# Performance work log

Measured on AMD Instinct MI355X. Metric: run time of the kernel, lower is better.

Reference implementation:

```python
import jax, jax.numpy as jnp
import numpy as np

N = 50000      # nodes
E = 800000     # edges
DIN = 256
DH = 256
DOUT = 64


def setup_inputs() -> dict:
    key = jax.random.key(0)
    ks = jax.random.split(key, 8)
    x = jax.random.normal(ks[0], (N, DIN), dtype=jnp.float32)
    edge_index = jax.random.randint(ks[1], (2, E), 0, N, dtype=jnp.int64)
    s = 0.05
    W1 = jax.random.normal(ks[2], (DIN, DH), dtype=jnp.float32) * s
    b1 = jnp.zeros((DH,), dtype=jnp.float32)
    W2 = jax.random.normal(ks[3], (DH, DH), dtype=jnp.float32) * s
    b2 = jnp.zeros((DH,), dtype=jnp.float32)
    W3 = jax.random.normal(ks[4], (DH, DOUT), dtype=jnp.float32) * s
    b3 = jnp.zeros((DOUT,), dtype=jnp.float32)
    return {"x": x, "edge_index": edge_index, "W1": W1, "b1": b1,
            "W2": W2, "b2": b2, "W3": W3, "b3": b3}


def gcn_conv(x, src, dst, deg_inv_sqrt, W, b):
    # x: [N, din] -> [N, dout]. PyG GCNConv: h = D^{-1/2}(A+I)D^{-1/2} (x W) + b
    n = x.shape[0]
    h = x @ W                                   # [N, dout]
    norm = deg_inv_sqrt[src] * deg_inv_sqrt[dst]  # [E+N]
    msgs = h[src] * norm[:, None]               # gather + scale, [E+N, dout]
    out = jax.ops.segment_sum(msgs, dst, num_segments=n)  # scatter-add
    return out + b


def _loops(edge_index, n):
    # add self loops, compute symmetric normalization degrees
    sl = jnp.arange(n, dtype=edge_index.dtype)
    src = jnp.concatenate([edge_index[0], sl])
    dst = jnp.concatenate([edge_index[1], sl])
    deg = jax.ops.segment_sum(jnp.ones_like(dst, dtype=jnp.float32), dst, num_segments=n)
    dis = jnp.where(deg > 0, jax.lax.rsqrt(deg), 0.0)
    return src, dst, dis


def reference(x, edge_index, W1, b1, W2, b2, W3, b3):
    src, dst, dis = _loops(edge_index, x.shape[0])
    h = jax.nn.relu(gcn_conv(x, src, dst, dis, W1, b1))   # dropout: eval no-op
    h = jax.nn.relu(gcn_conv(h, src, dst, dis, W2, b2))
    out = gcn_conv(h, src, dst, dis, W3, b3)              # batch=None -> no pooling
    return out
```

## Files before the change

kernel.cpp:

```cpp
#include <hip/hip_runtime.h>
#include <hip/hip_fp8.h>
#include <cstdint>
#include <cstddef>

typedef unsigned short u16;
typedef _Float16 f16x8 __attribute__((ext_vector_type(8)));
typedef float f32x2 __attribute__((ext_vector_type(2)));
typedef float f32x4 __attribute__((ext_vector_type(4)));

#if defined(__has_builtin)
#if __has_builtin(__builtin_amdgcn_cvt_pk_f32_fp8) && __has_builtin(__builtin_amdgcn_cvt_pk_fp8_f32)
#define FP8_BUILTIN 1
#endif
#endif

__device__ __forceinline__ float h2f(u16 u) {
  return (float)__builtin_bit_cast(_Float16, u);
}
__device__ __forceinline__ u16 f2h(float f) {
  return __builtin_bit_cast(u16, (_Float16)f);
}
__device__ __forceinline__ unsigned pkh(float lo, float hi) {
  return (unsigned)f2h(lo) | ((unsigned)f2h(hi) << 16);
}
__device__ __forceinline__ unsigned char ftofp8(float f) {
#ifdef FP8_BUILTIN
  return (unsigned char)(__builtin_amdgcn_cvt_pk_fp8_f32(f, f, 0, false) & 0xFF);
#else
  return __hip_fp8_e4m3(f).__x;
#endif
}

__device__ __forceinline__ void async16(u16* lds, const u16* g) {
  __builtin_amdgcn_global_load_lds(
      (const __attribute__((address_space(1))) unsigned int*)g,
      (__attribute__((address_space(3))) unsigned int*)lds, 16, 0, 0);
}

__device__ __forceinline__ void fma8p2(f32x2* a2, float d, uint2 p) {
#ifdef FP8_BUILTIN
  f32x2 d2; d2[0] = d; d2[1] = d;
  f32x2 v0 = __builtin_amdgcn_cvt_pk_f32_fp8((int)p.x, false);
  f32x2 v1 = __builtin_amdgcn_cvt_pk_f32_fp8((int)p.x, true);
  f32x2 v2 = __builtin_amdgcn_cvt_pk_f32_fp8((int)p.y, false);
  f32x2 v3 = __builtin_amdgcn_cvt_pk_f32_fp8((int)p.y, true);
  a2[0] += d2 * v0; a2[1] += d2 * v1; a2[2] += d2 * v2; a2[3] += d2 * v3;
#else
  const unsigned char* b = (const unsigned char*)&p;
#pragma unroll
  for (int k = 0; k < 8; ++k) {
    __hip_fp8_e4m3 v; v.__x = b[k];
    a2[k >> 1][k & 1] += d * (float)v;
  }
#endif
}

__device__ __forceinline__ void fma8h(float* a, float d, uint4 p) {
  const u16* q = (const u16*)&p;
#pragma unroll
  for (int k = 0; k < 8; ++k) a[k] += d * h2f(q[k]);
}

__device__ __forceinline__ f16x8 cvt8(const float* p) {
  float4 a = *(const float4*)p;
  float4 b = *(const float4*)(p + 4);
  f16x8 r;
  r[0] = (_Float16)a.x; r[1] = (_Float16)a.y; r[2] = (_Float16)a.z; r[3] = (_Float16)a.w;
  r[4] = (_Float16)b.x; r[5] = (_Float16)b.y; r[6] = (_Float16)b.z; r[7] = (_Float16)b.w;
  return r;
}

__device__ __forceinline__ int wave_is64(const void* ep) {
  const unsigned* p = (const unsigned*)ep;
  const int lane = threadIdx.x & 63;
  unsigned v = p[2 * lane + 1] | p[2 * (lane + 64) + 1];
  unsigned long long bal = __ballot(v != 0u);
  return (bal == 0ull) ? 1 : 0;
}

__device__ __forceinline__ int edge_at(const void* ep, int is64, long long idx) {
  if (is64) return (int)((const long long*)ep)[idx];
  return ((const int*)ep)[idx];
}

#define NCHUNK 256

__global__ void zero_f32(float* p, int n) {
  int i = blockIdx.x * 256 + threadIdx.x;
  if (i < n) p[i] = 0.f;
}

__global__ __launch_bounds__(256) void prep_all(
    const float* __restrict__ W1, u16* __restrict__ wt1,
    const float* __restrict__ W2, u16* __restrict__ wt2,
    const float* __restrict__ W3, u16* __restrict__ wt3,
    const void* __restrict__ ep, int* __restrict__ cnt,
    int E, int N, int DIN, int DH, int DOUT,
    int nb_w1, int nb_w2, int nb_w3) {
  int b = blockIdx.x;
  if (b < nb_w1) {
    int idx = b * 256 + threadIdx.x;
    if (idx < DIN * DH) {
      int n = idx / DIN, k = idx % DIN;
      wt1[idx] = f2h(W1[k * DH + n]);
    }
    return;
  }
  b -= nb_w1;
  if (b < nb_w2) {
    int idx = b * 256 + threadIdx.x;
    if (idx < DH * DH) {
      int n = idx / DH, k = idx % DH;
      wt2[idx] = f2h(W2[k * DH + n]);
    }
    return;
  }
  b -= nb_w2;
  if (b < nb_w3) {
    int idx = b * 256 + threadIdx.x;
    if (idx < DH * DOUT) {
      int n = idx / DH, k = idx % DH;
      wt3[idx] = f2h(W3[k * DOUT + n]);
    }
    return;
  }
  b -= nb_w3;
  {
    __shared__ int h[256];
    h[threadIdx.x] = 0;
    __syncthreads();
    int is64 = wave_is64(ep);
    const int per = (E + NCHUNK - 1) / NCHUNK;
    const int e0 = b * per, e1 = min(e0 + per, E);
    for (int e = e0 + (int)threadIdx.x; e < e1; e += 256) {
      int d = edge_at(ep, is64, (long long)E + e);
      d = min(max(d, 0), N - 1);
      atomicAdd(&h[d >> 8], 1);
    }
    __syncthreads();
    cnt[b * 256 + threadIdx.x] = h[threadIdx.x];
  }
}

__device__ __forceinline__ void bases_in_lds(const int* __restrict__ cnt,
                                             int nbuck, int E, int* bl, int* ws4) {
  const int t = threadIdx.x, lane = t & 63, w = t >> 6;
  int tot = 0;
  if (t < nbuck) {
#pragma unroll 4
    for (int c = 0; c < NCHUNK; ++c) tot += cnt[c * 256 + t];
  }
  int inc = tot;
#pragma unroll
  for (int o = 1; o < 64; o <<= 1) {
    int u = __shfl_up(inc, o, 64);
    if (lane >= o) inc += u;
  }
  if (lane == 63) ws4[w] = inc;
  __syncthreads();
  if (t == 0) {
    int run = 0;
#pragma unroll
    for (int k = 0; k < 4; ++k) { int v = ws4[k]; ws4[k + 4] = run; run += v; }
  }
  __syncthreads();
  bl[t] = ws4[w + 4] + inc - tot;
  if (t == 0) bl[nbuck] = E;
  __syncthreads();
}

__global__ __launch_bounds__(256) void csr_bucket(const void* __restrict__ ep,
                                                  const int* __restrict__ cnt,
                                                  unsigned* __restrict__ tmp,
                                                  int E, int N, int nbuck) {
  __shared__ int bl[257];
  __shared__ int cur[256];
  __shared__ int ws4[8];
  const int chunk = blockIdx.x;
  const int t = threadIdx.x;
  bases_in_lds(cnt, nbuck, E, bl, ws4);
  if (t < nbuck) {
    int partial = 0;
    for (int c = 0; c < chunk; ++c) partial += cnt[c * 256 + t];
    cur[t] = bl[t] + partial;
  }
  __syncthreads();
  int is64 = wave_is64(ep);
  const int per = (E + NCHUNK - 1) / NCHUNK;
  const int e0 = chunk * per, e1 = min(e0 + per, E);
  for (int e = e0 + t; e < e1; e += 256) {
    int s = edge_at(ep, is64, e);
    int d = edge_at(ep, is64, (long long)E + e);
    s = min(max(s, 0), N - 1);
    d = min(max(d, 0), N - 1);
    int pos = atomicAdd(&cur[d >> 8], 1);
    tmp[pos] = ((unsigned)d << 16) | (unsigned)s;
  }
}

__global__ __launch_bounds__(256) void csr_final(const unsigned* __restrict__ tmp,
                                                 const int* __restrict__ cnt,
                                                 int* __restrict__ rp,
                                                 float* __restrict__ dis,
                                                 u16* __restrict__ col,
                                                 int N, int E, int nbuck) {
  __shared__ int bl[257];
  __shared__ int hcnt[256];
  __shared__ int curs[256];
  __shared__ int ws4[8];
  const int b = blockIdx.x;
  const int node0 = b * 256;
  const int t = threadIdx.x, lane = t & 63, w = t >> 6;
  bases_in_lds(cnt, nbuck, E, bl, ws4);
  const int k0 = bl[b], k1 = bl[b + 1];
  hcnt[t] = 0;
  __syncthreads();
  for (int k = k0 + t; k < k1; k += 256)
    atomicAdd(&hcnt[(int)(tmp[k] >> 16) - node0], 1);
  __syncthreads();
  const int v = hcnt[t];
  int inc = v;
#pragma unroll
  for (int o = 1; o < 64; o <<= 1) {
    int u = __shfl_up(inc, o, 64);
    if (lane >= o) inc += u;
  }
  __syncthreads();
  if (lane == 63) ws4[w] = inc;
  __syncthreads();
  if (t == 0) {
    int run = 0;
#pragma unroll
    for (int k = 0; k < 4; ++k) { int vv = ws4[k]; ws4[k + 4] = run; run += vv; }
  }
  __syncthreads();
  const int excl = k0 + ws4[w + 4] + inc - v;
  if (node0 + t < N) {
    rp[node0 + t] = excl;
    dis[node0 + t] = rsqrtf((float)(v + 1));
  }
  if (b == 0 && t == 0) rp[N] = E;
  curs[t] = excl;
  __syncthreads();
  for (int k = k0 + t; k < k1; k += 256) {
    unsigned e = tmp[k];
    int dl = (int)(e >> 16) - node0;
    int pos = atomicAdd(&curs[dl], 1);
    col[pos] = (u16)(e & 0xFFFFu);
  }
}

template <int BN, int OUT8, int A32, int SC>
__global__ __launch_bounds__(256) void gemm_bres(const void* __restrict__ A,
                                                 const u16* __restrict__ Bt,
                                                 void* __restrict__ Cv, int Nt,
                                                 int Nrows) {
  constexpr int K = 256;
  constexpr int NJ = BN / 16;
  constexpr int CH = BN * K / 8;
  __shared__ __align__(16) u16 Bs[BN * K];

  const int tid = threadIdx.x, lane = tid & 63, w = tid >> 6;
  const int bm = blockIdx.x, bn = blockIdx.y;

#pragma unroll
  for (int i = 0; i < CH / 256; ++i) {
    int c = tid + i * 256;
    int ln = c & 63, t2 = c >> 6;
    int ks = t2 & 7, j = t2 >> 3;
    int row = j * 16 + (ln & 15);
    int kk = ks * 32 + (ln >> 4) * 8;
    async16(&Bs[(size_t)c * 8], Bt + (size_t)(bn * BN + row) * K + kk);
  }

  const int r16 = lane & 15, quad = lane >> 4;
  const int m0 = w * 32;

  int row0 = bm * 128 + m0 + r16;
  int row1 = row0 + 16;
  f16x8 aa0[8], aa1[8];
  if (A32) {
    row0 = min(row0, Nrows - 1);
    row1 = min(row1, Nrows - 1);
    const float* A0 = (const float*)A + (size_t)row0 * K + quad * 8;
    const float* A1 = (const float*)A + (size_t)row1 * K + quad * 8;
#pragma unroll
    for (int ks = 0; ks < 8; ++ks) {
      aa0[ks] = cvt8(A0 + ks * 32);
      aa1[ks] = cvt8(A1 + ks * 32);
    }
  } else {
    const u16* A0 = (const u16*)A + (size_t)row0 * K + quad * 8;
    const u16* A1 = (const u16*)A + (size_t)row1 * K + quad * 8;
#pragma unroll
    for (int ks = 0; ks < 8; ++ks) {
      aa0[ks] = *(const f16x8*)(A0 + ks * 32);
      aa1[ks] = *(const f16x8*)(A1 + ks * 32);
    }
  }

  f32x4 acc[2][NJ];
  const f32x4 fzero = {0.f, 0.f, 0.f, 0.f};
#pragma unroll
  for (int i = 0; i < 2; ++i)
#pragma unroll
    for (int j = 0; j < NJ; ++j) acc[i][j] = fzero;

  __syncthreads();

#pragma unroll
  for (int ks = 0; ks < 8; ++ks) {
#pragma unroll
    for (int j = 0; j < NJ; ++j) {
      f16x8 bf = *(const f16x8*)(&Bs[(size_t)((j * 8 + ks) * 64 + lane) * 8]);
      acc[0][j] = __builtin_amdgcn_mfma_f32_16x16x32_f16(aa0[ks], bf, acc[0][j], 0, 0, 0);
      acc[1][j] = __builtin_amdgcn_mfma_f32_16x16x32_f16(aa1[ks], bf, acc[1][j], 0, 0, 0);
    }
  }
#pragma unroll
  for (int i = 0; i < 2; ++i)
#pragma unroll
    for (int j = 0; j < NJ; ++j) {
      int gr = bm * 128 + m0 + i * 16 + quad * 4;
      int gc = bn * BN + j * 16 + r16;
#pragma unroll
      for (int r = 0; r < 4; ++r) {
        if (OUT8) {
          ((unsigned char*)Cv)[(size_t)(gr + r) * Nt + gc] =
              ftofp8(acc[i][j][r] * (float)SC);
        } else {
          ((u16*)Cv)[(size_t)(gr + r) * Nt + gc] = f2h(acc[i][j][r]);
        }
      }
    }
}

template <int SCALED>
__global__ __launch_bounds__(256) void agg_d256(const unsigned char* __restrict__ h,
                                                const int* __restrict__ rp,
                                                const u16* __restrict__ col,
                                                const float* __restrict__ dis,
                                                const float* __restrict__ bias,
                                                u16* __restrict__ out, int N) {
  const int wid = threadIdx.x >> 6, lane = threadIdx.x & 63;
  const int i = blockIdx.x * 4 + wid;
  if (i >= N) return;
  const int sub = lane >> 5;
  const int l32 = lane & 31;
  const int c8 = l32 * 8;
  const float di = dis[i];
  f32x2 a2[4];
#pragma unroll
  for (int k = 0; k < 4; ++k) { a2[k][0] = 0.f; a2[k][1] = 0.f; }
  if (sub == 0) {
    uint2 sv = *(const uint2*)(h + (size_t)i * 256 + c8);
    fma8p2(a2, SCALED ? 1.f : di, sv);
  }
  const int e1 = rp[i + 1];
  for (int base = rp[i]; base < e1; base += 64) {
    int me = base + lane;
    int s_l = 0; float d_l = 0.f;
    if (me < e1) { s_l = (int)col[me]; if (!SCALED) d_l = dis[s_l]; }
    const int cnt = min(64, e1 - base);
    const int cntR = (cnt + 7) & ~7;
    for (int t = 0; t < cntR; t += 8) {
      int sA = __shfl(s_l, t + sub, 64);
      int sB = __shfl(s_l, t + 2 + sub, 64);
      int sC = __shfl(s_l, t + 4 + sub, 64);
      int sD = __shfl(s_l, t + 6 + sub, 64);
      float dA, dB, dC, dD;
      if (SCALED) {
        dA = (t + sub < cnt) ? 1.f : 0.f;
        dB = (t + 2 + sub < cnt) ? 1.f : 0.f;
        dC = (t + 4 + sub < cnt) ? 1.f : 0.f;
        dD = (t + 6 + sub < cnt) ? 1.f : 0.f;
      } else {
        dA = __shfl(d_l, t + sub, 64);
        dB = __shfl(d_l, t + 2 + sub, 64);
        dC = __shfl(d_l, t + 4 + sub, 64);
        dD = __shfl(d_l, t + 6 + sub, 64);
      }
      uint2 pA = *(const uint2*)(h + (size_t)sA * 256 + c8);
      uint2 pB = *(const uint2*)(h + (size_t)sB * 256 + c8);
      uint2 pC = *(const uint2*)(h + (size_t)sC * 256 + c8);
      uint2 pD = *(const uint2*)(h + (size_t)sD * 256 + c8);
      fma8p2(a2, dA, pA); fma8p2(a2, dB, pB);
      fma8p2(a2, dC, pC); fma8p2(a2, dD, pD);
    }
  }
#pragma unroll
  for (int k = 0; k < 4; ++k) {
    a2[k][0] += __shfl_xor(a2[k][0], 32, 64);
    a2[k][1] += __shfl_xor(a2[k][1], 32, 64);
  }
  if (sub == 0) {
    const float inv = SCALED ? 0.25f : 1.f;
    float4 b0 = *(const float4*)(bias + c8);
    float4 b1 = *(const float4*)(bias + c8 + 4);
    float bb[8] = {b0.x, b0.y, b0.z, b0.w, b1.x, b1.y, b1.z, b1.w};
    float r[8];
#pragma unroll
    for (int k = 0; k < 8; ++k)
      r[k] = fmaxf(di * a2[k >> 1][k & 1] * inv + bb[k], 0.f) * di;
    uint4 ov;
    ov.x = pkh(r[0], r[1]); ov.y = pkh(r[2], r[3]);
    ov.z = pkh(r[4], r[5]); ov.w = pkh(r[6], r[7]);
    *(uint4*)(out + (size_t)i * 256 + c8) = ov;
  }
}

__global__ __launch_bounds__(256) void agg_d64(const u16* __restrict__ h,
                                               const int* __restrict__ rp,
                                               const u16* __restrict__ col,
                                               const float* __restrict__ dis,
                                               const float* __restrict__ bias,
                                               float* __restrict__ out, int N) {
  const int wid = threadIdx.x >> 6, lane = threadIdx.x & 63;
  const int i = blockIdx.x * 4 + wid;
  if (i >= N) return;
  const int grp = lane >> 3;
  const int l8 = lane & 7;
  const int c8 = l8 * 8;
  const float di = dis[i];
  float a[8] = {0.f, 0.f, 0.f, 0.f, 0.f, 0.f, 0.f, 0.f};
  if (grp == 0) {
    uint4 sv = *(const uint4*)(h + (size_t)i * 64 + c8);
    fma8h(a, 1.f, sv);
  }
  const int e1 = rp[i + 1];
  for (int base = rp[i]; base < e1; base += 64) {
    int me = base + lane;
    int s_l = 0;
    if (me < e1) s_l = (int)col[me];
    const int cnt = min(64, e1 - base);
    const int cntR = (cnt + 15) & ~15;
    for (int t = 0; t < cntR; t += 16) {
      int sA = __shfl(s_l, t + grp, 64);
      int sB = __shfl(s_l, t + 8 + grp, 64);
      float dA = (t + grp < cnt) ? 1.f : 0.f;
      float dB = (t + 8 + grp < cnt) ? 1.f : 0.f;
      uint4 pA = *(const uint4*)(h + (size_t)sA * 64 + c8);
      uint4 pB = *(const uint4*)(h + (size_t)sB * 64 + c8);
      fma8h(a, dA, pA); fma8h(a, dB, pB);
    }
  }
#pragma unroll
  for (int k = 0; k < 8; ++k) a[k] += __shfl_xor(a[k], 8, 64);
#pragma unroll
  for (int k = 0; k < 8; ++k) a[k] += __shfl_xor(a[k], 16, 64);
#pragma unroll
  for (int k = 0; k < 8; ++k) a[k] += __shfl_xor(a[k], 32, 64);
  if (lane < 8) {
    float4 b0 = *(const float4*)(bias + c8);
    float4 b1 = *(const float4*)(bias + c8 + 4);
    float4 o0, o1;
    o0.x = di * a[0] + b0.x; o0.y = di * a[1] + b0.y;
    o0.z = di * a[2] + b0.z; o0.w = di * a[3] + b0.w;
    o1.x = di * a[4] + b1.x; o1.y = di * a[5] + b1.y;
    o1.z = di * a[6] + b1.z; o1.w = di * a[7] + b1.w;
    *(float4*)(out + (size_t)i * 64 + c8) = o0;
    *(float4*)(out + (size_t)i * 64 + c8 + 4) = o1;
  }
}

extern "C" void kernel_launch(void* const* d_in, const int* in_sizes, int n_in,
                              void* d_out, int out_size, void* d_ws, size_t ws_size,
                              hipStream_t stream) {
  if (n_in < 8) return;
  const float* x = (const float*)d_in[0];
  const void* eptr = d_in[1];
  const float* W1 = (const float*)d_in[2];
  const float* b1 = (const float*)d_in[3];
  const float* W2 = (const float*)d_in[4];
  const float* b2 = (const float*)d_in[5];
  const float* W3 = (const float*)d_in[6];
  const float* b3 = (const float*)d_in[7];
  float* out = (float*)d_out;

  const int DIN = 256, DH = 256;
  const int N = in_sizes[0] / DIN;
  const int E = in_sizes[1] / 2;
  const int DOUT = in_sizes[6] / DH;
  const int MT = (N + 127) / 128;
  const int Mpad = MT * 128;
  const int nbuck = (N + 255) >> 8;

  auto rnd = [](size_t b) { return (b + 255) & ~(size_t)255; };
  size_t required = 0;
  required += rnd((size_t)Mpad * DH * 2);
  required += rnd((size_t)Mpad * DH);
  required += rnd((size_t)E * 2);
  required += rnd((size_t)E * 4);
  required += rnd((size_t)(N + 1) * 4);
  required += rnd((size_t)N * 4);
  required += rnd((size_t)DIN * DH * 2);
  required += rnd((size_t)DH * DH * 2);
  required += rnd((size_t)DH * DOUT * 2);
  required += rnd((size_t)256 * NCHUNK * 4);
  if (ws_size < required || N > 65536 || nbuck > 256 || nbuck < 1 ||
      E < 128 || DOUT != 64) {
    zero_f32<<<(out_size + 255) / 256, 256, 0, stream>>>(out, out_size);
    return;
  }

  char* ws = (char*)d_ws;
  size_t off0 = 0;
  auto alloc = [&](size_t bytes) {
    char* p = ws + off0;
    off0 = (off0 + bytes + 255) & ~(size_t)255;
    return p;
  };
  u16* xpad = (u16*)alloc((size_t)Mpad * DH * 2);
  unsigned char* hbuf = (unsigned char*)alloc((size_t)Mpad * DH);
  u16* colb = (u16*)alloc((size_t)E * 2);
  unsigned* tmpb = (unsigned*)alloc((size_t)E * 4);
  int* rp = (int*)alloc((size_t)(N + 1) * 4);
  float* dis = (float*)alloc((size_t)N * 4);
  u16* wt1 = (u16*)alloc((size_t)DIN * DH * 2);
  u16* wt2 = (u16*)alloc((size_t)DH * DH * 2);
  u16* wt3 = (u16*)alloc((size_t)DH * DOUT * 2);
  int* cnt = (int*)alloc((size_t)256 * NCHUNK * 4);

  const int nb_w1 = (DIN * DH + 255) / 256;
  const int nb_w2 = (DH * DH + 255) / 256;
  const int nb_w3 = (DH * DOUT + 255) / 256;
  prep_all<<<nb_w1 + nb_w2 + nb_w3 + NCHUNK, 256, 0, stream>>>(
      W1, wt1, W2, wt2, W3, wt3, eptr, cnt,
      E, N, DIN, DH, DOUT, nb_w1, nb_w2, nb_w3);

  csr_bucket<<<NCHUNK, 256, 0, stream>>>(eptr, cnt, tmpb, E, N, nbuck);
  csr_final<<<nbuck, 256, 0, stream>>>(tmpb, cnt, rp, dis, colb, N, E, nbuck);

  gemm_bres<128, 1, 1, 1><<<dim3(MT, DH / 128), 256, 0, stream>>>(
      x, wt1, hbuf, DH, N);
  agg_d256<0><<<(N + 3) / 4, 256, 0, stream>>>(hbuf, rp, colb, dis, b1, xpad, N);
  gemm_bres<128, 1, 0, 4><<<dim3(MT, DH / 128), 256, 0, stream>>>(
      xpad, wt2, hbuf, DH, N);
  agg_d256<1><<<(N + 3) / 4, 256, 0, stream>>>(hbuf, rp, colb, dis, b2, xpad, N);
  gemm_bres<64, 0, 0, 1><<<dim3(MT, DOUT / 64), 256, 0, stream>>>(
      xpad, wt3, hbuf, DOUT, N);
  agg_d64<<<(N + 3) / 4, 256, 0, stream>>>((const u16*)hbuf, rp, colb, dis, b3,
                                           out, N);
}
```

Before: 299.7 us.

## Loop GEMM over N tiles per block reusing A fragments; grid-stride aggregation kernels

```diff
diff --git a/kernel.cpp b/kernel.cpp
--- a/kernel.cpp
+++ b/kernel.cpp
@@ -250,32 +250,35 @@
   }
 }
 
-template <int BN, int OUT8, int A32, int SC>
-__global__ __launch_bounds__(256) void gemm_bres(const void* __restrict__ A,
-                                                 const u16* __restrict__ Bt,
-                                                 void* __restrict__ Cv, int Nt,
-                                                 int Nrows) {
+template <int OUT8, int A32, int NBT, int SC>
+__global__ __launch_bounds__(256) void gemm64c(const void* __restrict__ A,
+                                               const u16* __restrict__ Bt,
+                                               void* __restrict__ Cv, int Nt,
+                                               int Nrows) {
   constexpr int K = 256;
-  constexpr int NJ = BN / 16;
+  constexpr int BN = 64;
+  constexpr int NJ = 4;
   constexpr int CH = BN * K / 8;
   __shared__ __align__(16) u16 Bs[BN * K];
 
   const int tid = threadIdx.x, lane = tid & 63, w = tid >> 6;
-  const int bm = blockIdx.x, bn = blockIdx.y;
-
-#pragma unroll
-  for (int i = 0; i < CH / 256; ++i) {
-    int c = tid + i * 256;
-    int ln = c & 63, t2 = c >> 6;
-    int ks = t2 & 7, j = t2 >> 3;
-    int row = j * 16 + (ln & 15);
-    int kk = ks * 32 + (ln >> 4) * 8;
-    async16(&Bs[(size_t)c * 8], Bt + (size_t)(bn * BN + row) * K + kk);
-  }
+  const int bm = blockIdx.x;
+
+  auto stage = [&](int bt) {
+#pragma unroll
+    for (int i = 0; i < CH / 256; ++i) {
+      int c = tid + i * 256;
+      int ln = c & 63, t2 = c >> 6;
+      int ks = t2 & 7, j = t2 >> 3;
+      int row = bt * BN + j * 16 + (ln & 15);
+      int kk = ks * 32 + (ln >> 4) * 8;
+      async16(&Bs[(size_t)c * 8], Bt + (size_t)row * K + kk);
+    }
+  };
+  stage(0);
 
   const int r16 = lane & 15, quad = lane >> 4;
   const int m0 = w * 32;
-
   int row0 = bm * 128 + m0 + r16;
   int row1 = row0 + 16;
   f16x8 aa0[8], aa1[8];
@@ -299,40 +302,44 @@
     }
   }
 
-  f32x4 acc[2][NJ];
   const f32x4 fzero = {0.f, 0.f, 0.f, 0.f};
 #pragma unroll
-  for (int i = 0; i < 2; ++i)
-#pragma unroll
-    for (int j = 0; j < NJ; ++j) acc[i][j] = fzero;
-
-  __syncthreads();
-
-#pragma unroll
-  for (int ks = 0; ks < 8; ++ks) {
-#pragma unroll
-    for (int j = 0; j < NJ; ++j) {
-      f16x8 bf = *(const f16x8*)(&Bs[(size_t)((j * 8 + ks) * 64 + lane) * 8]);
-      acc[0][j] = __builtin_amdgcn_mfma_f32_16x16x32_f16(aa0[ks], bf, acc[0][j], 0, 0, 0);
-      acc[1][j] = __builtin_amdgcn_mfma_f32_16x16x32_f16(aa1[ks], bf, acc[1][j], 0, 0, 0);
-    }
-  }
-#pragma unroll
-  for (int i = 0; i < 2; ++i)
-#pragma unroll
-    for (int j = 0; j < NJ; ++j) {
-      int gr = bm * 128 + m0 + i * 16 + quad * 4;
-      int gc = bn * BN + j * 16 + r16;
-#pragma unroll
-      for (int r = 0; r < 4; ++r) {
-        if (OUT8) {
-          ((unsigned char*)Cv)[(size_t)(gr + r) * Nt + gc] =
-              ftofp8(acc[i][j][r] * (float)SC);
-        } else {
-          ((u16*)Cv)[(size_t)(gr + r) * Nt + gc] = f2h(acc[i][j][r]);
+  for (int bt = 0; bt < NBT; ++bt) {
+    f32x4 acc[2][NJ];
+#pragma unroll
+    for (int i = 0; i < 2; ++i)
+#pragma unroll
+      for (int j = 0; j < NJ; ++j) acc[i][j] = fzero;
+    __syncthreads();
+#pragma unroll
+    for (int ks = 0; ks < 8; ++ks)
+#pragma unroll
+      for (int j = 0; j < NJ; ++j) {
+        f16x8 bf = *(const f16x8*)(&Bs[(size_t)((j * 8 + ks) * 64 + lane) * 8]);
+        acc[0][j] = __builtin_amdgcn_mfma_f32_16x16x32_f16(aa0[ks], bf, acc[0][j], 0, 0, 0);
+        acc[1][j] = __builtin_amdgcn_mfma_f32_16x16x32_f16(aa1[ks], bf, acc[1][j], 0, 0, 0);
+      }
+    if (bt + 1 < NBT) {
+      __syncthreads();
+      stage(bt + 1);
+    }
+#pragma unroll
+    for (int i = 0; i < 2; ++i)
+#pragma unroll
+      for (int j = 0; j < NJ; ++j) {
+        int gr = bm * 128 + m0 + i * 16 + quad * 4;
+        int gc = bt * BN + j * 16 + r16;
+#pragma unroll
+        for (int r = 0; r < 4; ++r) {
+          if (OUT8) {
+            ((unsigned char*)Cv)[(size_t)(gr + r) * Nt + gc] =
+                ftofp8(acc[i][j][r] * (float)SC);
+          } else {
+            ((u16*)Cv)[(size_t)(gr + r) * Nt + gc] = f2h(acc[i][j][r]);
+          }
         }
       }
-    }
+  }
 }
 
 template <int SCALED>
@@ -343,69 +350,70 @@
                                                 const float* __restrict__ bias,
                                                 u16* __restrict__ out, int N) {
   const int wid = threadIdx.x >> 6, lane = threadIdx.x & 63;
-  const int i = blockIdx.x * 4 + wid;
-  if (i >= N) return;
   const int sub = lane >> 5;
   const int l32 = lane & 31;
   const int c8 = l32 * 8;
-  const float di = dis[i];
-  f32x2 a2[4];
-#pragma unroll
-  for (int k = 0; k < 4; ++k) { a2[k][0] = 0.f; a2[k][1] = 0.f; }
-  if (sub == 0) {
-    uint2 sv = *(const uint2*)(h + (size_t)i * 256 + c8);
-    fma8p2(a2, SCALED ? 1.f : di, sv);
-  }
-  const int e1 = rp[i + 1];
-  for (int base = rp[i]; base < e1; base += 64) {
-    int me = base + lane;
-    int s_l = 0; float d_l = 0.f;
-    if (me < e1) { s_l = (int)col[me]; if (!SCALED) d_l = dis[s_l]; }
-    const int cnt = min(64, e1 - base);
-    const int cntR = (cnt + 7) & ~7;
-    for (int t = 0; t < cntR; t += 8) {
-      int sA = __shfl(s_l, t + sub, 64);
-      int sB = __shfl(s_l, t + 2 + sub, 64);
-      int sC = __shfl(s_l, t + 4 + sub, 64);
-      int sD = __shfl(s_l, t + 6 + sub, 64);
-      float dA, dB, dC, dD;
-      if (SCALED) {
-        dA = (t + sub < cnt) ? 1.f : 0.f;
-        dB = (t + 2 + sub < cnt) ? 1.f : 0.f;
-        dC = (t + 4 + sub < cnt) ? 1.f : 0.f;
-        dD = (t + 6 + sub < cnt) ? 1.f : 0.f;
-      } else {
-        dA = __shfl(d_l, t + sub, 64);
-        dB = __shfl(d_l, t + 2 + sub, 64);
-        dC = __shfl(d_l, t + 4 + sub, 64);
-        dD = __shfl(d_l, t + 6 + sub, 64);
+  const int stride = gridDim.x * 4;
+  for (int i = blockIdx.x * 4 + wid; i < N; i += stride) {
+    const float di = dis[i];
+    f32x2 a2[4];
+#pragma unroll
+    for (int k = 0; k < 4; ++k) { a2[k][0] = 0.f; a2[k][1] = 0.f; }
+    if (sub == 0) {
+      uint2 sv = *(const uint2*)(h + (size_t)i * 256 + c8);
+      fma8p2(a2, SCALED ? 1.f : di, sv);
+    }
+    const int e1 = rp[i + 1];
+    for (int base = rp[i]; base < e1; base += 64) {
+      int me = base + lane;
+      int s_l = 0; float d_l = 0.f;
+      if (me < e1) { s_l = (int)col[me]; if (!SCALED) d_l = dis[s_l]; }
+      const int cnt = min(64, e1 - base);
+      const int cntR = (cnt + 7) & ~7;
+      for (int t = 0; t < cntR; t += 8) {
+        int sA = __shfl(s_l, t + sub, 64);
+        int sB = __shfl(s_l, t + 2 + sub, 64);
+        int sC = __shfl(s_l, t + 4 + sub, 64);
+        int sD = __shfl(s_l, t + 6 + sub, 64);
+        float dA, dB, dC, dD;
+        if (SCALED) {
+          dA = (t + sub < cnt) ? 1.f : 0.f;
+          dB = (t + 2 + sub < cnt) ? 1.f : 0.f;
+          dC = (t + 4 + sub < cnt) ? 1.f : 0.f;
+          dD = (t + 6 + sub < cnt) ? 1.f : 0.f;
+        } else {
+          dA = __shfl(d_l, t + sub, 64);
+          dB = __shfl(d_l, t + 2 + sub, 64);
+          dC = __shfl(d_l, t + 4 + sub, 64);
+          dD = __shfl(d_l, t + 6 + sub, 64);
+        }
+        uint2 pA = *(const uint2*)(h + (size_t)sA * 256 + c8);
+        uint2 pB = *(const uint2*)(h + (size_t)sB * 256 + c8);
+        uint2 pC = *(const uint2*)(h + (size_t)sC * 256 + c8);
+        uint2 pD = *(const uint2*)(h + (size_t)sD * 256 + c8);
+        fma8p2(a2, dA, pA); fma8p2(a2, dB, pB);
+        fma8p2(a2, dC, pC); fma8p2(a2, dD, pD);
       }
-      uint2 pA = *(const uint2*)(h + (size_t)sA * 256 + c8);
-      uint2 pB = *(const uint2*)(h + (size_t)sB * 256 + c8);
-      uint2 pC = *(const uint2*)(h + (size_t)sC * 256 + c8);
-      uint2 pD = *(const uint2*)(h + (size_t)sD * 256 + c8);
-      fma8p2(a2, dA, pA); fma8p2(a2, dB, pB);
-      fma8p2(a2, dC, pC); fma8p2(a2, dD, pD);
-    }
-  }
-#pragma unroll
-  for (int k = 0; k < 4; ++k) {
-    a2[k][0] += __shfl_xor(a2[k][0], 32, 64);
-    a2[k][1] += __shfl_xor(a2[k][1], 32, 64);
-  }
-  if (sub == 0) {
-    const float inv = SCALED ? 0.25f : 1.f;
-    float4 b0 = *(const float4*)(bias + c8);
-    float4 b1 = *(const float4*)(bias + c8 + 4);
-    float bb[8] = {b0.x, b0.y, b0.z, b0.w, b1.x, b1.y, b1.z, b1.w};
-    float r[8];
-#pragma unroll
-    for (int k = 0; k < 8; ++k)
-      r[k] = fmaxf(di * a2[k >> 1][k & 1] * inv + bb[k], 0.f) * di;
-    uint4 ov;
-    ov.x = pkh(r[0], r[1]); ov.y = pkh(r[2], r[3]);
-    ov.z = pkh(r[4], r[5]); ov.w = pkh(r[6], r[7]);
-    *(uint4*)(out + (size_t)i * 256 + c8) = ov;
+    }
+#pragma unroll
+    for (int k = 0; k < 4; ++k) {
+      a2[k][0] += __shfl_xor(a2[k][0], 32, 64);
+      a2[k][1] += __shfl_xor(a2[k][1], 32, 64);
+    }
+    if (sub == 0) {
+      const float inv = SCALED ? 0.25f : 1.f;
+      float4 b0 = *(const float4*)(bias + c8);
+      float4 b1 = *(const float4*)(bias + c8 + 4);
+      float bb[8] = {b0.x, b0.y, b0.z, b0.w, b1.x, b1.y, b1.z, b1.w};
+      float r[8];
+#pragma unroll
+      for (int k = 0; k < 8; ++k)
+        r[k] = fmaxf(di * a2[k >> 1][k & 1] * inv + bb[k], 0.f) * di;
+      uint4 ov;
+      ov.x = pkh(r[0], r[1]); ov.y = pkh(r[2], r[3]);
+      ov.z = pkh(r[4], r[5]); ov.w = pkh(r[6], r[7]);
+      *(uint4*)(out + (size_t)i * 256 + c8) = ov;
+    }
   }
 }
 
@@ -416,50 +424,51 @@
                                                const float* __restrict__ bias,
                                                float* __restrict__ out, int N) {
   const int wid = threadIdx.x >> 6, lane = threadIdx.x & 63;
-  const int i = blockIdx.x * 4 + wid;
-  if (i >= N) return;
   const int grp = lane >> 3;
   const int l8 = lane & 7;
   const int c8 = l8 * 8;
-  const float di = dis[i];
-  float a[8] = {0.f, 0.f, 0.f, 0.f, 0.f, 0.f, 0.f, 0.f};
-  if (grp == 0) {
-    uint4 sv = *(const uint4*)(h + (size_t)i * 64 + c8);
-    fma8h(a, 1.f, sv);
-  }
-  const int e1 = rp[i + 1];
-  for (int base = rp[i]; base < e1; base += 64) {
-    int me = base + lane;
-    int s_l = 0;
-    if (me < e1) s_l = (int)col[me];
-    const int cnt = min(64, e1 - base);
-    const int cntR = (cnt + 15) & ~15;
-    for (int t = 0; t < cntR; t += 16) {
-      int sA = __shfl(s_l, t + grp, 64);
-      int sB = __shfl(s_l, t + 8 + grp, 64);
-      float dA = (t + grp < cnt) ? 1.f : 0.f;
-      float dB = (t + 8 + grp < cnt) ? 1.f : 0.f;
-      uint4 pA = *(const uint4*)(h + (size_t)sA * 64 + c8);
-      uint4 pB = *(const uint4*)(h + (size_t)sB * 64 + c8);
-      fma8h(a, dA, pA); fma8h(a, dB, pB);
-    }
-  }
-#pragma unroll
-  for (int k = 0; k < 8; ++k) a[k] += __shfl_xor(a[k], 8, 64);
-#pragma unroll
-  for (int k = 0; k < 8; ++k) a[k] += __shfl_xor(a[k], 16, 64);
-#pragma unroll
-  for (int k = 0; k < 8; ++k) a[k] += __shfl_xor(a[k], 32, 64);
-  if (lane < 8) {
-    float4 b0 = *(const float4*)(bias + c8);
-    float4 b1 = *(const float4*)(bias + c8 + 4);
-    float4 o0, o1;
-    o0.x = di * a[0] + b0.x; o0.y = di * a[1] + b0.y;
-    o0.z = di * a[2] + b0.z; o0.w = di * a[3] + b0.w;
-    o1.x = di * a[4] + b1.x; o1.y = di * a[5] + b1.y;
-    o1.z = di * a[6] + b1.z; o1.w = di * a[7] + b1.w;
-    *(float4*)(out + (size_t)i * 64 + c8) = o0;
-    *(float4*)(out + (size_t)i * 64 + c8 + 4) = o1;
+  const int stride = gridDim.x * 4;
+  for (int i = blockIdx.x * 4 + wid; i < N; i += stride) {
+    const float di = dis[i];
+    float a[8] = {0.f, 0.f, 0.f, 0.f, 0.f, 0.f, 0.f, 0.f};
+    if (grp == 0) {
+      uint4 sv = *(const uint4*)(h + (size_t)i * 64 + c8);
+      fma8h(a, 1.f, sv);
+    }
+    const int e1 = rp[i + 1];
+    for (int base = rp[i]; base < e1; base += 64) {
+      int me = base + lane;
+      int s_l = 0;
+      if (me < e1) s_l = (int)col[me];
+      const int cnt = min(64, e1 - base);
+      const int cntR = (cnt + 15) & ~15;
+      for (int t = 0; t < cntR; t += 16) {
+        int sA = __shfl(s_l, t + grp, 64);
+        int sB = __shfl(s_l, t + 8 + grp, 64);
+        float dA = (t + grp < cnt) ? 1.f : 0.f;
+        float dB = (t + 8 + grp < cnt) ? 1.f : 0.f;
+        uint4 pA = *(const uint4*)(h + (size_t)sA * 64 + c8);
+        uint4 pB = *(const uint4*)(h + (size_t)sB * 64 + c8);
+        fma8h(a, dA, pA); fma8h(a, dB, pB);
+      }
+    }
+#pragma unroll
+    for (int k = 0; k < 8; ++k) a[k] += __shfl_xor(a[k], 8, 64);
+#pragma unroll
+    for (int k = 0; k < 8; ++k) a[k] += __shfl_xor(a[k], 16, 64);
+#pragma unroll
+    for (int k = 0; k < 8; ++k) a[k] += __shfl_xor(a[k], 32, 64);
+    if (lane < 8) {
+      float4 b0 = *(const float4*)(bias + c8);
+      float4 b1 = *(const float4*)(bias + c8 + 4);
+      float4 o0, o1;
+      o0.x = di * a[0] + b0.x; o0.y = di * a[1] + b0.y;
+      o0.z = di * a[2] + b0.z; o0.w = di * a[3] + b0.w;
+      o1.x = di * a[4] + b1.x; o1.y = di * a[5] + b1.y;
+      o1.z = di * a[6] + b1.z; o1.w = di * a[7] + b1.w;
+      *(float4*)(out + (size_t)i * 64 + c8) = o0;
+      *(float4*)(out + (size_t)i * 64 + c8 + 4) = o1;
+    }
   }
 }
 
@@ -531,14 +540,12 @@
   csr_bucket<<<NCHUNK, 256, 0, stream>>>(eptr, cnt, tmpb, E, N, nbuck);
   csr_final<<<nbuck, 256, 0, stream>>>(tmpb, cnt, rp, dis, colb, N, E, nbuck);
 
-  gemm_bres<128, 1, 1, 1><<<dim3(MT, DH / 128), 256, 0, stream>>>(
-      x, wt1, hbuf, DH, N);
-  agg_d256<0><<<(N + 3) / 4, 256, 0, stream>>>(hbuf, rp, colb, dis, b1, xpad, N);
-  gemm_bres<128, 1, 0, 4><<<dim3(MT, DH / 128), 256, 0, stream>>>(
-      xpad, wt2, hbuf, DH, N);
-  agg_d256<1><<<(N + 3) / 4, 256, 0, stream>>>(hbuf, rp, colb, dis, b2, xpad, N);
-  gemm_bres<64, 0, 0, 1><<<dim3(MT, DOUT / 64), 256, 0, stream>>>(
-      xpad, wt3, hbuf, DOUT, N);
-  agg_d64<<<(N + 3) / 4, 256, 0, stream>>>((const u16*)hbuf, rp, colb, dis, b3,
-                                           out, N);
-}
+  const int gb = min((N + 3) / 4, 2048);
+
+  gemm64c<1, 1, 4, 1><<<MT, 256, 0, stream>>>(x, wt1, hbuf, DH, N);
+  agg_d256<0><<<gb, 256, 0, stream>>>(hbuf, rp, colb, dis, b1, xpad, N);
+  gemm64c<1, 0, 4, 4><<<MT, 256, 0, stream>>>(xpad, wt2, hbuf, DH, N);
+  agg_d256<1><<<gb, 256, 0, stream>>>(hbuf, rp, colb, dis, b2, xpad, N);
+  gemm64c<0, 0, 1, 1><<<MT, 256, 0, stream>>>(xpad, wt3, hbuf, DOUT, N);
+  agg_d64<<<gb, 256, 0, stream>>>((const u16*)hbuf, rp, colb, dis, b3, out, N);
+}
```

Result: slower. 305.9 us (+2.1%).
